# Performance work log

Measured on AMD Instinct MI355X. Metric: run time of the kernel, lower is better.

## Reference

```python
import jax, jax.numpy as jnp
import numpy as np

NUM_HEADS = 16
ROPE_THETA = 10000.0


def apply_rope(x):
    # x: (B, H, T, hd), interleaved-pair RoPE (rotary-embedding-torch convention)
    T, hd = x.shape[-2], x.shape[-1]
    inv_freq = 1.0 / (ROPE_THETA ** (jnp.arange(0, hd, 2, dtype=jnp.float32) / hd))  # (hd/2,)
    ang = jnp.arange(T, dtype=jnp.float32)[:, None] * inv_freq[None, :]  # (T, hd/2)
    cos, sin = jnp.cos(ang), jnp.sin(ang)
    x1 = x[..., 0::2]
    x2 = x[..., 1::2]
    r1 = x1 * cos - x2 * sin
    r2 = x1 * sin + x2 * cos
    return jnp.stack([r1, r2], axis=-1).reshape(x.shape)


def setup_inputs() -> dict:
    key = jax.random.key(0)
    ks = jax.random.split(key, 8)
    L, S, B, E = 2048, 2048, 2, 1024
    sc = 1.0 / np.sqrt(E)
    return {
        "query": jax.random.normal(ks[0], (L, B, E), jnp.float32),
        "key": jax.random.normal(ks[1], (S, B, E), jnp.float32),
        "value": jax.random.normal(ks[2], (S, B, E), jnp.float32),
        "key_padding_mask": jnp.zeros((B, S), dtype=bool),
        "Wq": jax.random.normal(ks[3], (E, E), jnp.float32) * sc,
        "bq": jnp.zeros((E,), jnp.float32),
        "Wk": jax.random.normal(ks[4], (E, E), jnp.float32) * sc,
        "bk": jnp.zeros((E,), jnp.float32),
        "Wv": jax.random.normal(ks[5], (E, E), jnp.float32) * sc,
        "bv": jnp.zeros((E,), jnp.float32),
        "Wo": jax.random.normal(ks[6], (E, E), jnp.float32) * sc,
        "bo": jnp.zeros((E,), jnp.float32),
    }


def reference(query, key, value, key_padding_mask, Wq, bq, Wk, bk, Wv, bv, Wo, bo):
    L, B, E = query.shape
    S = key.shape[0]
    H = NUM_HEADS
    hd = E // H
    # projections (torch Linear: x @ W.T + b)
    Q = query @ Wq.T + bq  # (L, B, E)
    K = key @ Wk.T + bk    # (S, B, E)
    V = value @ Wv.T + bv  # (S, B, E)
    # (T, B, E) -> (B, H, T, hd)
    Q = Q.reshape(L, B, H, hd).transpose(1, 2, 0, 3)
    K = K.reshape(S, B, H, hd).transpose(1, 2, 0, 3)
    V = V.reshape(S, B, H, hd).transpose(1, 2, 0, 3)
    Q = apply_rope(Q)
    K = apply_rope(K)
    scores = jnp.einsum("bhld,bhsd->bhls", Q, K) / jnp.sqrt(jnp.float32(hd))
    scores = jnp.where(key_padding_mask[:, None, None, :], -jnp.inf, scores)
    attn = jax.nn.softmax(scores, axis=-1)
    out = jnp.einsum("bhls,bhsd->bhld", attn, V)  # (B, H, L, hd)
    out = out.transpose(2, 0, 1, 3).reshape(L, B, E)
    return out @ Wo.T + bo
```

## Files before the change

kernel.cpp:

```cpp
#include <hip/hip_runtime.h>
#include <hip/hip_bf16.h>

typedef __hip_bfloat16 bf16;
typedef short bf16x8 __attribute__((ext_vector_type(8)));
typedef float f32x4 __attribute__((ext_vector_type(4)));
typedef short s4 __attribute__((ext_vector_type(4)));

#define LL 2048
#define SS 2048
#define EE 1024
#define HH 16
#define HD 64
#define MM (LL * 2)

static __device__ __forceinline__ short f2bs(float f) {
  bf16 h = __float2bfloat16(f);
  short u;
  __builtin_memcpy(&u, &h, 2);
  return u;
}

static __device__ __forceinline__ void st8(bf16* p, float4 x, float4 y) {
  bf16x8 v;
  v[0] = f2bs(x.x); v[1] = f2bs(x.y); v[2] = f2bs(x.z); v[3] = f2bs(x.w);
  v[4] = f2bs(y.x); v[5] = f2bs(y.y); v[6] = f2bs(y.z); v[7] = f2bs(y.w);
  *(bf16x8*)p = v;
}

#define GLL16(gp, lp) __builtin_amdgcn_global_load_lds(                        \
    (const __attribute__((address_space(1))) void*)(gp),                       \
    (__attribute__((address_space(3))) void*)(lp), 16, 0, 0)

__global__ __launch_bounds__(256) void prep_kernel(
    float2* __restrict__ tab, const unsigned char* __restrict__ m,
    float* __restrict__ mf,
    const float* __restrict__ s0, const float* __restrict__ s1,
    const float* __restrict__ s2, const float* __restrict__ s3,
    bf16* __restrict__ wdst, float* __restrict__ zout) {
  const int bid = blockIdx.x;
  if (bid < 256) {
    int i = bid * 256 + threadIdx.x;
    int pos = i >> 5, fi = i & 31;
    float freq = expf(-(float)fi * (9.210340371976184f / 32.0f));
    float ang = (float)pos * freq;
    float s, c;
    sincosf(ang, &s, &c);
    tab[i] = make_float2(c, s);
  } else if (bid < 272) {
    int i = (bid - 256) * 256 + threadIdx.x;
    if (i < 2 * SS) mf[i] = m[i] ? -1e30f : 0.f;
  } else if (bid < 4368) {
    int b2 = bid - 272;
    int sel = b2 >> 10;
    const float* src = (sel == 0) ? s0 : (sel == 1) ? s1 : (sel == 2) ? s2 : s3;
    size_t loc = ((size_t)(b2 & 1023) * 256 + threadIdx.x) * 4;
    float4 v = *(const float4*)(src + loc);
    s4 p;
    p[0] = f2bs(v.x); p[1] = f2bs(v.y); p[2] = f2bs(v.z); p[3] = f2bs(v.w);
    *(s4*)(wdst + (size_t)sel * EE * EE + loc) = p;
  } else {
    size_t i = ((size_t)(bid - 4368) * 256 + threadIdx.x) * 4;
    *(float4*)(zout + i) = make_float4(0.f, 0.f, 0.f, 0.f);
  }
}

template<int MODE, bool XB16, bool WB16>
__global__ __launch_bounds__(256) void proj_kernel(
    const void* __restrict__ Xv, const void* __restrict__ Wv,
    const float* __restrict__ bias, void* __restrict__ dstv,
    const float2* __restrict__ tab)
{
  const int w = threadIdx.x >> 6;
  const int lane = threadIdx.x & 63;
  const int l15 = lane & 15, quad = lane >> 4;
  const int tm = blockIdx.x * 128 + w * 32;
  const int tn = blockIdx.y * 64;

  const size_t aoff0 = (size_t)(tm + l15) * EE + quad * 8;
  const size_t aoff1 = aoff0 + (size_t)16 * EE;
  const size_t woff  = (size_t)(tn + l15) * EE + quad * 8;

  f32x4 zero4 = {0.f, 0.f, 0.f, 0.f};
  f32x4 acc[2][4];
#pragma unroll
  for (int mi = 0; mi < 2; ++mi)
#pragma unroll
    for (int ni = 0; ni < 4; ++ni) acc[mi][ni] = zero4;

  for (int k0 = 0; k0 < EE; k0 += 32) {
    bf16x8 a0, a1;
    if (XB16 || MODE == 3) {
      const bf16* Xb = (const bf16*)Xv;
      a0 = *(const bf16x8*)(Xb + aoff0 + k0);
      a1 = *(const bf16x8*)(Xb + aoff1 + k0);
    } else {
      const float* Xf = (const float*)Xv;
#pragma unroll
      for (int j = 0; j < 8; ++j) a0[j] = f2bs(Xf[aoff0 + k0 + j]);
#pragma unroll
      for (int j = 0; j < 8; ++j) a1[j] = f2bs(Xf[aoff1 + k0 + j]);
    }
#pragma unroll
    for (int ni = 0; ni < 4; ++ni) {
      bf16x8 bv;
      if (WB16) {
        const bf16* Wb = (const bf16*)Wv;
        bv = *(const bf16x8*)(Wb + woff + (size_t)ni * 16 * EE + k0);
      } else {
        const float* Wf = (const float*)Wv;
#pragma unroll
        for (int j = 0; j < 8; ++j) bv[j] = f2bs(Wf[woff + (size_t)ni * 16 * EE + k0 + j]);
      }
      acc[0][ni] = __builtin_amdgcn_mfma_f32_16x16x32_bf16(a0, bv, acc[0][ni], 0, 0, 0);
      acc[1][ni] = __builtin_amdgcn_mfma_f32_16x16x32_bf16(a1, bv, acc[1][ni], 0, 0, 0);
    }
  }

  float bz[4];
#pragma unroll
  for (int ni = 0; ni < 4; ++ni) bz[ni] = bias[tn + ni * 16 + l15];

#pragma unroll
  for (int mi = 0; mi < 2; ++mi) {
#pragma unroll
    for (int ni = 0; ni < 4; ++ni) {
      const int n = tn + ni * 16 + l15;
#pragma unroll
      for (int r = 0; r < 4; ++r) {
        const int m = tm + mi * 16 + quad * 4 + r;
        float v = acc[mi][ni][r] + bz[ni];
        if (MODE <= 1) {
          float other = __shfl_xor(v, 1, 64);
          int pos = m >> 1, b = m & 1, d = n & 63, h = n >> 6;
          float2 cs = tab[pos * 32 + (d >> 1)];
          float rv = (d & 1) ? (other * cs.y + v * cs.x) : (v * cs.x - other * cs.y);
          ((bf16*)dstv)[((size_t)(b * HH + h) * LL + pos) * HD + d] = __float2bfloat16(rv);
        } else if (MODE == 2) {
          int pos = m >> 1, b = m & 1, d = n & 63, h = n >> 6;
          ((bf16*)dstv)[((size_t)(b * HH + h) * HD + d) * SS + pos] = __float2bfloat16(v);
        } else {
          ((float*)dstv)[(size_t)m * EE + n] = v;
        }
      }
    }
  }
}

__global__ __launch_bounds__(256, 6) void qkv_kernel(
    const float* __restrict__ Xq, const float* __restrict__ Xk,
    const float* __restrict__ Xv, const bf16* __restrict__ Wb,
    const float* __restrict__ bq, const float* __restrict__ bk,
    const float* __restrict__ bv, bf16* __restrict__ Qr,
    bf16* __restrict__ Kr, bf16* __restrict__ Vt,
    const float2* __restrict__ tab)
{
  __shared__ __align__(16) bf16 As[2][128 * 32];
  __shared__ __align__(16) bf16 Bs[2][64 * 32];

  const int tid = threadIdx.x;
  const int w = tid >> 6;
  const int lane = tid & 63;
  const int l15 = lane & 15, quad = lane >> 4;
  const int id = blockIdx.x;
  const int z = id >> 9;
  const int g = id & 511;
  const int tmb = (g & 31) * 128;
  const int tn  = (g >> 5) * 64;

  const float* Xf = (z == 0) ? Xq : (z == 1) ? Xk : Xv;
  const bf16* Wm  = Wb + (size_t)z * EE * EE;
  const float* bias = (z == 0) ? bq : (z == 1) ? bk : bv;
  bf16* dst = (z == 0) ? Qr : (z == 1) ? Kr : Vt;

  const int ar = tid >> 2;
  const int ac = (tid & 3) * 8;
  const float* gA0 = Xf + (size_t)(tmb + ar) * EE + ac;
  const float* gA1 = gA0 + (size_t)64 * EE;
  const bf16* gB = Wm + (size_t)(tn + w * 16 + (lane >> 2)) * EE + (lane & 3) * 8;

  f32x4 zero4 = {0.f, 0.f, 0.f, 0.f};
  f32x4 acc[2][4];
#pragma unroll
  for (int mi = 0; mi < 2; ++mi)
#pragma unroll
    for (int ni = 0; ni < 4; ++ni) acc[mi][ni] = zero4;

  {
    float4 a00 = *(const float4*)(gA0);
    float4 a01 = *(const float4*)(gA0 + 4);
    float4 a10 = *(const float4*)(gA1);
    float4 a11 = *(const float4*)(gA1 + 4);
    GLL16(gB, (bf16*)&Bs[0][w * 16 * 32] + lane * 8);
    st8(&As[0][ar * 32 + ac], a00, a01);
    st8(&As[0][(64 + ar) * 32 + ac], a10, a11);
  }
  __syncthreads();

  for (int t = 0; t < 32; ++t) {
    const int cur = t & 1;
    float4 a00, a01, a10, a11;
    if (t < 31) {
      const int k0 = (t + 1) * 32;
      a00 = *(const float4*)(gA0 + k0);
      a01 = *(const float4*)(gA0 + k0 + 4);
      a10 = *(const float4*)(gA1 + k0);
      a11 = *(const float4*)(gA1 + k0 + 4);
      GLL16(gB + k0, (bf16*)&Bs[cur ^ 1][w * 16 * 32] + lane * 8);
    }
    bf16x8 af0 = *(const bf16x8*)(&As[cur][(w * 32 + l15) * 32 + quad * 8]);
    bf16x8 af1 = *(const bf16x8*)(&As[cur][(w * 32 + 16 + l15) * 32 + quad * 8]);
#pragma unroll
    for (int ni = 0; ni < 4; ++ni) {
      bf16x8 bfr = *(const bf16x8*)(&Bs[cur][(ni * 16 + l15) * 32 + quad * 8]);
      acc[0][ni] = __builtin_amdgcn_mfma_f32_16x16x32_bf16(af0, bfr, acc[0][ni], 0, 0, 0);
      acc[1][ni] = __builtin_amdgcn_mfma_f32_16x16x32_bf16(af1, bfr, acc[1][ni], 0, 0, 0);
    }
    if (t < 31) {
      st8(&As[cur ^ 1][ar * 32 + ac], a00, a01);
      st8(&As[cur ^ 1][(64 + ar) * 32 + ac], a10, a11);
    }
    __syncthreads();
  }

  float bz[4];
#pragma unroll
  for (int ni = 0; ni < 4; ++ni) bz[ni] = bias[tn + ni * 16 + l15];

#pragma unroll
  for (int mi = 0; mi < 2; ++mi) {
#pragma unroll
    for (int ni = 0; ni < 4; ++ni) {
      const int n = tn + ni * 16 + l15;
#pragma unroll
      for (int r = 0; r < 4; ++r) {
        const int m = tmb + w * 32 + mi * 16 + quad * 4 + r;
        float v = acc[mi][ni][r] + bz[ni];
        if (z <= 1) {
          float other = __shfl_xor(v, 1, 64);
          int pos = m >> 1, b = m & 1, d = n & 63, h = n >> 6;
          float2 cs = tab[pos * 32 + (d >> 1)];
          float rv = (d & 1) ? (other * cs.y + v * cs.x) : (v * cs.x - other * cs.y);
          dst[((size_t)(b * HH + h) * LL + pos) * HD + d] = __float2bfloat16(rv);
        } else {
          int pos = m >> 1, b = m & 1, d = n & 63, h = n >> 6;
          dst[((size_t)(b * HH + h) * HD + d) * SS + pos] = __float2bfloat16(v);
        }
      }
    }
  }
}

__global__ __launch_bounds__(256, 8) void projo_kernel(
    const bf16* __restrict__ X, const bf16* __restrict__ W,
    const float* __restrict__ bias, float* __restrict__ dst)
{
  __shared__ __align__(16) bf16 As[2][64 * 32];
  __shared__ __align__(16) bf16 Bs[2][64 * 32];

  const int tid = threadIdx.x;
  const int w = tid >> 6;
  const int lane = tid & 63;
  const int l15 = lane & 15, quad = lane >> 4;
  const int tmb = blockIdx.x * 64;
  const int tn  = blockIdx.y * 64;
  const int kb  = blockIdx.z * 512;

  const bf16* gA = X + (size_t)(tmb + w * 16 + (lane >> 2)) * EE + kb + (lane & 3) * 8;
  const bf16* gB = W + (size_t)(tn  + w * 16 + (lane >> 2)) * EE + kb + (lane & 3) * 8;

  f32x4 zero4 = {0.f, 0.f, 0.f, 0.f};
  f32x4 acc[4];
#pragma unroll
  for (int ni = 0; ni < 4; ++ni) acc[ni] = zero4;

  GLL16(gA, (bf16*)&As[0][w * 16 * 32] + lane * 8);
  GLL16(gB, (bf16*)&Bs[0][w * 16 * 32] + lane * 8);
  __syncthreads();

  for (int t = 0; t < 16; ++t) {
    const int cur = t & 1;
    if (t < 15) {
      const int k0 = (t + 1) * 32;
      GLL16(gA + k0, (bf16*)&As[cur ^ 1][w * 16 * 32] + lane * 8);
      GLL16(gB + k0, (bf16*)&Bs[cur ^ 1][w * 16 * 32] + lane * 8);
    }
    bf16x8 af = *(const bf16x8*)(&As[cur][(w * 16 + l15) * 32 + quad * 8]);
#pragma unroll
    for (int ni = 0; ni < 4; ++ni) {
      bf16x8 bfr = *(const bf16x8*)(&Bs[cur][(ni * 16 + l15) * 32 + quad * 8]);
      acc[ni] = __builtin_amdgcn_mfma_f32_16x16x32_bf16(af, bfr, acc[ni], 0, 0, 0);
    }
    __syncthreads();
  }

  float bz[4];
#pragma unroll
  for (int ni = 0; ni < 4; ++ni)
    bz[ni] = (blockIdx.z == 0) ? bias[tn + ni * 16 + l15] : 0.f;

#pragma unroll
  for (int ni = 0; ni < 4; ++ni) {
    const int n = tn + ni * 16 + l15;
#pragma unroll
    for (int r = 0; r < 4; ++r) {
      const int m = tmb + w * 16 + quad * 4 + r;
      atomicAdd(&dst[(size_t)m * EE + n], acc[ni][r] + bz[ni]);
    }
  }
}

__global__ __launch_bounds__(256) void attn_kernel(
    const bf16* __restrict__ Qr, const bf16* __restrict__ Kr,
    const bf16* __restrict__ Vt, const float* __restrict__ maskf,
    bf16* __restrict__ ctx)
{
  __shared__ __align__(16) bf16 Ks[2][64 * 64];
  __shared__ __align__(16) bf16 Vs[2][64 * 64];
  __shared__ __align__(16) short Plds[4][32][56];

  const int w = threadIdx.x >> 6;
  const int lane = threadIdx.x & 63;
  const int l15 = lane & 15, quad = lane >> 4;
  const int id = blockIdx.x;
  const int bh = id & 31;
  const int qt = id >> 5;
  const int b = bh >> 4, h = bh & 15;
  const int q0 = qt * 128 + w * 32;

  const bf16* Qbh = Qr + (size_t)bh * LL * HD;
  const bf16* Kbh = Kr + (size_t)bh * SS * HD;
  const bf16* Vbh = Vt + (size_t)bh * HD * SS;
  const float* mrow = maskf + b * SS;

  bf16x8 qf[2][2];
#pragma unroll
  for (int mi = 0; mi < 2; ++mi) {
    const bf16* qp = Qbh + (size_t)(q0 + mi * 16 + l15) * HD + quad * 8;
    qf[mi][0] = *(const bf16x8*)(qp);
    qf[mi][1] = *(const bf16x8*)(qp + 32);
  }

  const int srow = lane >> 3;
  const int gswz = ((lane & 7) ^ srow) * 8;
  const int kswz0 = ((quad    ) ^ (l15 & 7)) * 8;
  const int kswz1 = ((quad + 4) ^ (l15 & 7)) * 8;

#define STAGE(buf, S0) {                                                       \
    _Pragma("unroll")                                                          \
    for (int i = 0; i < 2; ++i) {                                              \
      const int rb = w * 16 + i * 8;                                           \
      GLL16(Kbh + (size_t)((S0) + rb + srow) * HD + gswz,                      \
            (bf16*)&Ks[buf][rb * 64] + lane * 8);                              \
      GLL16(Vbh + (size_t)(rb + srow) * SS + (S0) + gswz,                      \
            (bf16*)&Vs[buf][rb * 64] + lane * 8);                              \
    }                                                                          \
  }

  f32x4 zero4 = {0.f, 0.f, 0.f, 0.f};
  f32x4 o[2][4];
#pragma unroll
  for (int mi = 0; mi < 2; ++mi)
#pragma unroll
    for (int t = 0; t < 4; ++t) o[mi][t] = zero4;
  float ps0 = 0.f, ps1 = 0.f;

  STAGE(0, 0);
  __syncthreads();

  for (int t = 0; t < SS / 64; ++t) {
    const int s0 = t * 64;
    const int cur = t & 1;
    if (t + 1 < SS / 64) STAGE(cur ^ 1, s0 + 64);

#pragma unroll
    for (int ss = 0; ss < 2; ++ss) {
      const bf16* Kb = &Ks[cur][ss * 32 * 64];
      bf16x8 kf00 = *(const bf16x8*)(Kb + (l15)      * 64 + kswz0);
      bf16x8 kf01 = *(const bf16x8*)(Kb + (l15)      * 64 + kswz1);
      bf16x8 kf10 = *(const bf16x8*)(Kb + (16 + l15) * 64 + kswz0);
      bf16x8 kf11 = *(const bf16x8*)(Kb + (16 + l15) * 64 + kswz1);
      bf16x8 vf[4];
#pragma unroll
      for (int tt = 0; tt < 4; ++tt)
        vf[tt] = *(const bf16x8*)(&Vs[cur][0] + (tt * 16 + l15) * 64 +
                                  (((ss * 4 + quad) ^ (l15 & 7)) * 8));
      f32x4 mv0 = *(const f32x4*)(mrow + s0 + ss * 32 + quad * 4);
      f32x4 mv1 = *(const f32x4*)(mrow + s0 + ss * 32 + 16 + quad * 4);

#pragma unroll
      for (int mi = 0; mi < 2; ++mi) {
        f32x4 sc0 = zero4, sc1 = zero4;
        sc0 = __builtin_amdgcn_mfma_f32_16x16x32_bf16(kf00, qf[mi][0], sc0, 0, 0, 0);
        sc0 = __builtin_amdgcn_mfma_f32_16x16x32_bf16(kf01, qf[mi][1], sc0, 0, 0, 0);
        sc1 = __builtin_amdgcn_mfma_f32_16x16x32_bf16(kf10, qf[mi][0], sc1, 0, 0, 0);
        sc1 = __builtin_amdgcn_mfma_f32_16x16x32_bf16(kf11, qf[mi][1], sc1, 0, 0, 0);
        s4 pk0, pk1;
#pragma unroll
        for (int r = 0; r < 4; ++r) {
          float p = __expf(sc0[r] * 0.125f + mv0[r]);
          if (mi == 0) ps0 += p; else ps1 += p;
          pk0[r] = f2bs(p);
        }
#pragma unroll
        for (int r = 0; r < 4; ++r) {
          float p = __expf(sc1[r] * 0.125f + mv1[r]);
          if (mi == 0) ps0 += p; else ps1 += p;
          pk1[r] = f2bs(p);
        }
        *(s4*)&Plds[w][mi * 16 + l15][quad * 4] = pk0;
        *(s4*)&Plds[w][mi * 16 + l15][16 + quad * 4] = pk1;
      }
      asm volatile("" ::: "memory");
      bf16x8 pf0 = *(const bf16x8*)&Plds[w][l15][quad * 8];
      bf16x8 pf1 = *(const bf16x8*)&Plds[w][16 + l15][quad * 8];
#pragma unroll
      for (int tt = 0; tt < 4; ++tt) {
        o[0][tt] = __builtin_amdgcn_mfma_f32_16x16x32_bf16(pf0, vf[tt], o[0][tt], 0, 0, 0);
        o[1][tt] = __builtin_amdgcn_mfma_f32_16x16x32_bf16(pf1, vf[tt], o[1][tt], 0, 0, 0);
      }
      asm volatile("" ::: "memory");
    }
    __syncthreads();
  }
#undef STAGE

  float lv0 = ps0; lv0 += __shfl_xor(lv0, 16, 64); lv0 += __shfl_xor(lv0, 32, 64);
  float lv1 = ps1; lv1 += __shfl_xor(lv1, 16, 64); lv1 += __shfl_xor(lv1, 32, 64);

#pragma unroll
  for (int mi = 0; mi < 2; ++mi) {
#pragma unroll
    for (int r = 0; r < 4; ++r) {
      float lv = (mi == 0) ? lv0 : lv1;
      float li = __shfl(lv, quad * 4 + r, 64);
      float inv = 1.0f / li;
      int q = q0 + mi * 16 + quad * 4 + r;
#pragma unroll
      for (int t = 0; t < 4; ++t) {
        float val = o[mi][t][r] * inv;
        ctx[(size_t)(q * 2 + b) * EE + (size_t)h * 64 + t * 16 + l15] = __float2bfloat16(val);
      }
    }
  }
}

extern "C" void kernel_launch(void* const* d_in, const int* in_sizes, int n_in,
                              void* d_out, int out_size, void* d_ws, size_t ws_size,
                              hipStream_t stream) {
  const float* query = (const float*)d_in[0];
  const float* key   = (const float*)d_in[1];
  const float* value = (const float*)d_in[2];
  const unsigned char* mask = (const unsigned char*)d_in[3];
  const float* Wq = (const float*)d_in[4];
  const float* bq = (const float*)d_in[5];
  const float* Wk = (const float*)d_in[6];
  const float* bk = (const float*)d_in[7];
  const float* Wv = (const float*)d_in[8];
  const float* bv = (const float*)d_in[9];
  const float* Wo = (const float*)d_in[10];
  const float* bo = (const float*)d_in[11];

  char* ws = (char*)d_ws;
  const bool big = ws_size >= ((size_t)41 << 20);

  float2* tab   = (float2*)ws;
  float*  maskf = (float*)(ws + (512 << 10));
  bf16* Wb = (bf16*)(ws + ((size_t)1 << 20));
  size_t base = big ? ((size_t)9 << 20) : ((size_t)1 << 20);
  bf16* Qr  = (bf16*)(ws + base);
  bf16* Kr  = (bf16*)(ws + base + ((size_t)8 << 20));
  bf16* Vt  = (bf16*)(ws + base + ((size_t)16 << 20));
  bf16* ctx = (bf16*)(ws + base + ((size_t)24 << 20));

  prep_kernel<<<big ? 8464 : 272, 256, 0, stream>>>(
      tab, mask, maskf, Wq, Wk, Wv, Wo, Wb, (float*)d_out);

  if (big) {
    qkv_kernel<<<1536, 256, 0, stream>>>(query, key, value, Wb, bq, bk, bv,
                                         Qr, Kr, Vt, tab);
  } else {
    dim3 gp(MM / 128, EE / 64);
    proj_kernel<0, false, false><<<gp, 256, 0, stream>>>(query, Wq, bq, Qr, tab);
    proj_kernel<1, false, false><<<gp, 256, 0, stream>>>(key,   Wk, bk, Kr, tab);
    proj_kernel<2, false, false><<<gp, 256, 0, stream>>>(value, Wv, bv, Vt, tab);
  }

  attn_kernel<<<(LL / 128) * 2 * HH, 256, 0, stream>>>(Qr, Kr, Vt, maskf, ctx);

  if (big) {
    dim3 go(MM / 64, EE / 64, 2);
    projo_kernel<<<go, 256, 0, stream>>>(ctx, Wb + (size_t)3 * EE * EE, bo, (float*)d_out);
  } else {
    dim3 gp(MM / 128, EE / 64);
    proj_kernel<3, true, false><<<gp, 256, 0, stream>>>(ctx, Wo, bo, d_out, tab);
  }
}
```

Baseline: 277.5 us.

## Enlarge QKV GEMM tiles, swizzle LDS, drop split-K atomics in output projection

The QKV projection kernel now computes 128x128 tiles per block, with each wave owning a 64x64 sub-tile (4x4 MFMAs) and XOR-swizzled LDS layouts, halving the grid. The output projection drops its split-K over two z-slices and atomicAdd, using K-steps of 64 with swizzled LDS and plain stores. This also removes the zero-fill of the output from the prep kernel. The aim is more reuse per loaded tile, fewer LDS bank conflicts and no atomic traffic, at the cost of fewer blocks, more registers and lower occupancy.

```diff
diff --git a/kernel.cpp b/kernel.cpp
--- a/kernel.cpp
+++ b/kernel.cpp
@@ -36,7 +36,7 @@
     float* __restrict__ mf,
     const float* __restrict__ s0, const float* __restrict__ s1,
     const float* __restrict__ s2, const float* __restrict__ s3,
-    bf16* __restrict__ wdst, float* __restrict__ zout) {
+    bf16* __restrict__ wdst) {
   const int bid = blockIdx.x;
   if (bid < 256) {
     int i = bid * 256 + threadIdx.x;
@@ -49,7 +49,7 @@
   } else if (bid < 272) {
     int i = (bid - 256) * 256 + threadIdx.x;
     if (i < 2 * SS) mf[i] = m[i] ? -1e30f : 0.f;
-  } else if (bid < 4368) {
+  } else {
     int b2 = bid - 272;
     int sel = b2 >> 10;
     const float* src = (sel == 0) ? s0 : (sel == 1) ? s1 : (sel == 2) ? s2 : s3;
@@ -58,9 +58,6 @@
     s4 p;
     p[0] = f2bs(v.x); p[1] = f2bs(v.y); p[2] = f2bs(v.z); p[3] = f2bs(v.w);
     *(s4*)(wdst + (size_t)sel * EE * EE + loc) = p;
-  } else {
-    size_t i = ((size_t)(bid - 4368) * 256 + threadIdx.x) * 4;
-    *(float4*)(zout + i) = make_float4(0.f, 0.f, 0.f, 0.f);
   }
 }
 
@@ -146,7 +143,7 @@
   }
 }
 
-__global__ __launch_bounds__(256, 6) void qkv_kernel(
+__global__ __launch_bounds__(256, 3) void qkv_kernel(
     const float* __restrict__ Xq, const float* __restrict__ Xk,
     const float* __restrict__ Xv, const bf16* __restrict__ Wb,
     const float* __restrict__ bq, const float* __restrict__ bk,
@@ -154,18 +151,18 @@
     bf16* __restrict__ Kr, bf16* __restrict__ Vt,
     const float2* __restrict__ tab)
 {
-  __shared__ __align__(16) bf16 As[2][128 * 32];
-  __shared__ __align__(16) bf16 Bs[2][64 * 32];
+  __shared__ __align__(16) bf16 As[2][4096];
+  __shared__ __align__(16) bf16 Bs[2][4096];
 
   const int tid = threadIdx.x;
   const int w = tid >> 6;
   const int lane = tid & 63;
   const int l15 = lane & 15, quad = lane >> 4;
   const int id = blockIdx.x;
-  const int z = id >> 9;
-  const int g = id & 511;
+  const int z = id >> 8;
+  const int g = id & 255;
   const int tmb = (g & 31) * 128;
-  const int tn  = (g >> 5) * 64;
+  const int tn  = (g >> 5) * 128;
 
   const float* Xf = (z == 0) ? Xq : (z == 1) ? Xk : Xv;
   const bf16* Wm  = Wb + (size_t)z * EE * EE;
@@ -173,15 +170,25 @@
   bf16* dst = (z == 0) ? Qr : (z == 1) ? Kr : Vt;
 
   const int ar = tid >> 2;
-  const int ac = (tid & 3) * 8;
-  const float* gA0 = Xf + (size_t)(tmb + ar) * EE + ac;
+  const int akc = tid & 3;
+  const float* gA0 = Xf + (size_t)(tmb + ar) * EE + akc * 8;
   const float* gA1 = gA0 + (size_t)64 * EE;
-  const bf16* gB = Wm + (size_t)(tn + w * 16 + (lane >> 2)) * EE + (lane & 3) * 8;
+  const int aw0 = (ar >> 1) * 64 + (((((ar & 1) << 2) | akc) ^ ((ar >> 1) & 7)) * 8);
+  const int aw1 = aw0 + 2048;
+
+  const int ub = (lane & 7) ^ (lane >> 3);
+  const bf16* gB0 = Wm + (size_t)(tn + w * 32 + 2 * (lane >> 3) + (ub >> 2)) * EE
+                       + (ub & 3) * 8;
+  const bf16* gB1 = gB0 + (size_t)16 * EE;
+
+  const int arbase = (l15 >> 1) * 64 + (((((l15 & 1) << 2) | quad) ^ (l15 >> 1)) * 8);
+  const int wmh = (w >> 1) * 2048;
+  const int wnh = (w & 1) * 2048;
 
   f32x4 zero4 = {0.f, 0.f, 0.f, 0.f};
-  f32x4 acc[2][4];
-#pragma unroll
-  for (int mi = 0; mi < 2; ++mi)
+  f32x4 acc[4][4];
+#pragma unroll
+  for (int mi = 0; mi < 4; ++mi)
 #pragma unroll
     for (int ni = 0; ni < 4; ++ni) acc[mi][ni] = zero4;
 
@@ -190,9 +197,10 @@
     float4 a01 = *(const float4*)(gA0 + 4);
     float4 a10 = *(const float4*)(gA1);
     float4 a11 = *(const float4*)(gA1 + 4);
-    GLL16(gB, (bf16*)&Bs[0][w * 16 * 32] + lane * 8);
-    st8(&As[0][ar * 32 + ac], a00, a01);
-    st8(&As[0][(64 + ar) * 32 + ac], a10, a11);
+    GLL16(gB0, (bf16*)&Bs[0][w * 1024] + lane * 8);
+    GLL16(gB1, (bf16*)&Bs[0][w * 1024 + 512] + lane * 8);
+    st8(&As[0][aw0], a00, a01);
+    st8(&As[0][aw1], a10, a11);
   }
   __syncthreads();
 
@@ -205,35 +213,41 @@
       a01 = *(const float4*)(gA0 + k0 + 4);
       a10 = *(const float4*)(gA1 + k0);
       a11 = *(const float4*)(gA1 + k0 + 4);
-      GLL16(gB + k0, (bf16*)&Bs[cur ^ 1][w * 16 * 32] + lane * 8);
-    }
-    bf16x8 af0 = *(const bf16x8*)(&As[cur][(w * 32 + l15) * 32 + quad * 8]);
-    bf16x8 af1 = *(const bf16x8*)(&As[cur][(w * 32 + 16 + l15) * 32 + quad * 8]);
+      GLL16(gB0 + k0, (bf16*)&Bs[cur ^ 1][w * 1024] + lane * 8);
+      GLL16(gB1 + k0, (bf16*)&Bs[cur ^ 1][w * 1024 + 512] + lane * 8);
+    }
+    bf16x8 af[4], bfr[4];
+#pragma unroll
+    for (int mi = 0; mi < 4; ++mi)
+      af[mi] = *(const bf16x8*)(&As[cur][wmh + mi * 512 + arbase]);
+#pragma unroll
+    for (int ni = 0; ni < 4; ++ni)
+      bfr[ni] = *(const bf16x8*)(&Bs[cur][wnh + ni * 512 + arbase]);
+#pragma unroll
+    for (int mi = 0; mi < 4; ++mi)
+#pragma unroll
+      for (int ni = 0; ni < 4; ++ni)
+        acc[mi][ni] = __builtin_amdgcn_mfma_f32_16x16x32_bf16(af[mi], bfr[ni], acc[mi][ni], 0, 0, 0);
+    if (t < 31) {
+      st8(&As[cur ^ 1][aw0], a00, a01);
+      st8(&As[cur ^ 1][aw1], a10, a11);
+    }
+    __syncthreads();
+  }
+
+  const int wm = (w >> 1) * 64, wn = (w & 1) * 64;
+  float bz[4];
+#pragma unroll
+  for (int ni = 0; ni < 4; ++ni) bz[ni] = bias[tn + wn + ni * 16 + l15];
+
+#pragma unroll
+  for (int mi = 0; mi < 4; ++mi) {
 #pragma unroll
     for (int ni = 0; ni < 4; ++ni) {
-      bf16x8 bfr = *(const bf16x8*)(&Bs[cur][(ni * 16 + l15) * 32 + quad * 8]);
-      acc[0][ni] = __builtin_amdgcn_mfma_f32_16x16x32_bf16(af0, bfr, acc[0][ni], 0, 0, 0);
-      acc[1][ni] = __builtin_amdgcn_mfma_f32_16x16x32_bf16(af1, bfr, acc[1][ni], 0, 0, 0);
-    }
-    if (t < 31) {
-      st8(&As[cur ^ 1][ar * 32 + ac], a00, a01);
-      st8(&As[cur ^ 1][(64 + ar) * 32 + ac], a10, a11);
-    }
-    __syncthreads();
-  }
-
-  float bz[4];
-#pragma unroll
-  for (int ni = 0; ni < 4; ++ni) bz[ni] = bias[tn + ni * 16 + l15];
-
-#pragma unroll
-  for (int mi = 0; mi < 2; ++mi) {
-#pragma unroll
-    for (int ni = 0; ni < 4; ++ni) {
-      const int n = tn + ni * 16 + l15;
+      const int n = tn + wn + ni * 16 + l15;
 #pragma unroll
       for (int r = 0; r < 4; ++r) {
-        const int m = tmb + w * 32 + mi * 16 + quad * 4 + r;
+        const int m = tmb + wm + mi * 16 + quad * 4 + r;
         float v = acc[mi][ni][r] + bz[ni];
         if (z <= 1) {
           float other = __shfl_xor(v, 1, 64);
@@ -250,12 +264,12 @@
   }
 }
 
-__global__ __launch_bounds__(256, 8) void projo_kernel(
+__global__ __launch_bounds__(256, 4) void projo_kernel(
     const bf16* __restrict__ X, const bf16* __restrict__ W,
     const float* __restrict__ bias, float* __restrict__ dst)
 {
-  __shared__ __align__(16) bf16 As[2][64 * 32];
-  __shared__ __align__(16) bf16 Bs[2][64 * 32];
+  __shared__ __align__(16) bf16 As[2][4096];
+  __shared__ __align__(16) bf16 Bs[2][4096];
 
   const int tid = threadIdx.x;
   const int w = tid >> 6;
@@ -263,40 +277,51 @@
   const int l15 = lane & 15, quad = lane >> 4;
   const int tmb = blockIdx.x * 64;
   const int tn  = blockIdx.y * 64;
-  const int kb  = blockIdx.z * 512;
-
-  const bf16* gA = X + (size_t)(tmb + w * 16 + (lane >> 2)) * EE + kb + (lane & 3) * 8;
-  const bf16* gB = W + (size_t)(tn  + w * 16 + (lane >> 2)) * EE + kb + (lane & 3) * 8;
+
+  const int u8 = ((lane & 7) ^ (lane >> 3)) * 8;
+  const bf16* gA0 = X + (size_t)(tmb + w * 16 + (lane >> 3)) * EE + u8;
+  const bf16* gA1 = gA0 + (size_t)8 * EE;
+  const bf16* gB0 = W + (size_t)(tn + w * 16 + (lane >> 3)) * EE + u8;
+  const bf16* gB1 = gB0 + (size_t)8 * EE;
+
+  const int asw0 = ((quad    ) ^ (l15 & 7)) * 8;
+  const int asw1 = ((quad + 4) ^ (l15 & 7)) * 8;
 
   f32x4 zero4 = {0.f, 0.f, 0.f, 0.f};
   f32x4 acc[4];
 #pragma unroll
   for (int ni = 0; ni < 4; ++ni) acc[ni] = zero4;
 
-  GLL16(gA, (bf16*)&As[0][w * 16 * 32] + lane * 8);
-  GLL16(gB, (bf16*)&Bs[0][w * 16 * 32] + lane * 8);
+  GLL16(gA0, (bf16*)&As[0][(w * 16) * 64] + lane * 8);
+  GLL16(gA1, (bf16*)&As[0][(w * 16 + 8) * 64] + lane * 8);
+  GLL16(gB0, (bf16*)&Bs[0][(w * 16) * 64] + lane * 8);
+  GLL16(gB1, (bf16*)&Bs[0][(w * 16 + 8) * 64] + lane * 8);
   __syncthreads();
 
   for (int t = 0; t < 16; ++t) {
     const int cur = t & 1;
     if (t < 15) {
-      const int k0 = (t + 1) * 32;
-      GLL16(gA + k0, (bf16*)&As[cur ^ 1][w * 16 * 32] + lane * 8);
-      GLL16(gB + k0, (bf16*)&Bs[cur ^ 1][w * 16 * 32] + lane * 8);
-    }
-    bf16x8 af = *(const bf16x8*)(&As[cur][(w * 16 + l15) * 32 + quad * 8]);
+      const int k0 = (t + 1) * 64;
+      GLL16(gA0 + k0, (bf16*)&As[cur ^ 1][(w * 16) * 64] + lane * 8);
+      GLL16(gA1 + k0, (bf16*)&As[cur ^ 1][(w * 16 + 8) * 64] + lane * 8);
+      GLL16(gB0 + k0, (bf16*)&Bs[cur ^ 1][(w * 16) * 64] + lane * 8);
+      GLL16(gB1 + k0, (bf16*)&Bs[cur ^ 1][(w * 16 + 8) * 64] + lane * 8);
+    }
+    bf16x8 a0 = *(const bf16x8*)(&As[cur][(w * 16 + l15) * 64 + asw0]);
+    bf16x8 a1 = *(const bf16x8*)(&As[cur][(w * 16 + l15) * 64 + asw1]);
 #pragma unroll
     for (int ni = 0; ni < 4; ++ni) {
-      bf16x8 bfr = *(const bf16x8*)(&Bs[cur][(ni * 16 + l15) * 32 + quad * 8]);
-      acc[ni] = __builtin_amdgcn_mfma_f32_16x16x32_bf16(af, bfr, acc[ni], 0, 0, 0);
+      bf16x8 b0 = *(const bf16x8*)(&Bs[cur][(ni * 16 + l15) * 64 + asw0]);
+      bf16x8 b1 = *(const bf16x8*)(&Bs[cur][(ni * 16 + l15) * 64 + asw1]);
+      acc[ni] = __builtin_amdgcn_mfma_f32_16x16x32_bf16(a0, b0, acc[ni], 0, 0, 0);
+      acc[ni] = __builtin_amdgcn_mfma_f32_16x16x32_bf16(a1, b1, acc[ni], 0, 0, 0);
     }
     __syncthreads();
   }
 
   float bz[4];
 #pragma unroll
-  for (int ni = 0; ni < 4; ++ni)
-    bz[ni] = (blockIdx.z == 0) ? bias[tn + ni * 16 + l15] : 0.f;
+  for (int ni = 0; ni < 4; ++ni) bz[ni] = bias[tn + ni * 16 + l15];
 
 #pragma unroll
   for (int ni = 0; ni < 4; ++ni) {
@@ -304,7 +329,7 @@
 #pragma unroll
     for (int r = 0; r < 4; ++r) {
       const int m = tmb + w * 16 + quad * 4 + r;
-      atomicAdd(&dst[(size_t)m * EE + n], acc[ni][r] + bz[ni]);
+      dst[(size_t)m * EE + n] = acc[ni][r] + bz[ni];
     }
   }
 }
@@ -472,12 +497,12 @@
   bf16* Vt  = (bf16*)(ws + base + ((size_t)16 << 20));
   bf16* ctx = (bf16*)(ws + base + ((size_t)24 << 20));
 
-  prep_kernel<<<big ? 8464 : 272, 256, 0, stream>>>(
-      tab, mask, maskf, Wq, Wk, Wv, Wo, Wb, (float*)d_out);
+  prep_kernel<<<big ? 4368 : 272, 256, 0, stream>>>(
+      tab, mask, maskf, Wq, Wk, Wv, Wo, Wb);
 
   if (big) {
-    qkv_kernel<<<1536, 256, 0, stream>>>(query, key, value, Wb, bq, bk, bv,
-                                         Qr, Kr, Vt, tab);
+    qkv_kernel<<<768, 256, 0, stream>>>(query, key, value, Wb, bq, bk, bv,
+                                        Qr, Kr, Vt, tab);
   } else {
     dim3 gp(MM / 128, EE / 64);
     proj_kernel<0, false, false><<<gp, 256, 0, stream>>>(query, Wq, bq, Qr, tab);
@@ -488,7 +513,7 @@
   attn_kernel<<<(LL / 128) * 2 * HH, 256, 0, stream>>>(Qr, Kr, Vt, maskf, ctx);
 
   if (big) {
-    dim3 go(MM / 64, EE / 64, 2);
+    dim3 go(MM / 64, EE / 64);
     projo_kernel<<<go, 256, 0, stream>>>(ctx, Wb + (size_t)3 * EE * EE, bo, (float*)d_out);
   } else {
     dim3 gp(MM / 128, EE / 64);
```

Result: faster. 271.4 us (-2.2%).
